# Performance work log

Hardware: AMD Instinct MI355X
Metric: run time of the kernel (lower is better)

The kernel has to match this reference:

```python
import jax, jax.numpy as jnp
import numpy as np

EMBED_DIM = 1024


def setup_inputs() -> dict:
    key = jax.random.key(0)
    ks = jax.random.split(key, 9)
    d = EMBED_DIM
    s = 1.0 / np.sqrt(d)
    x = jax.random.normal(ks[0], (4, 4096, d), dtype=jnp.float32)
    Wq = jax.random.normal(ks[1], (d, d), dtype=jnp.float32) * s
    bq = jax.random.normal(ks[2], (d,), dtype=jnp.float32) * 0.01
    Wk = jax.random.normal(ks[3], (d, d), dtype=jnp.float32) * s
    bk = jax.random.normal(ks[4], (d,), dtype=jnp.float32) * 0.01
    Wv = jax.random.normal(ks[5], (d, d), dtype=jnp.float32) * s
    bv = jax.random.normal(ks[6], (d,), dtype=jnp.float32) * 0.01
    Wo = jax.random.normal(ks[7], (d, d), dtype=jnp.float32) * s
    bo = jax.random.normal(ks[8], (d,), dtype=jnp.float32) * 0.01
    return {"x": x, "Wq": Wq, "bq": bq, "Wk": Wk, "bk": bk,
            "Wv": Wv, "bv": bv, "Wo": Wo, "bo": bo}


def reference(x, Wq, bq, Wk, bk, Wv, bv, Wo, bo):
    # x: [b, s, d]; single-head attention, scale = 1/sqrt(d)
    b, s, d = x.shape
    q = x @ Wq + bq
    k = x @ Wk + bk
    v = x @ Wv + bv
    scale = 1.0 / jnp.sqrt(jnp.asarray(d, x.dtype))
    scores = jnp.einsum('bqd,bkd->bqk', q, k) * scale  # [b, s, s]
    causal = jnp.tril(jnp.ones((s, s), dtype=bool))
    scores = jnp.where(causal, scores, jnp.asarray(-jnp.inf, scores.dtype))
    attn = jax.nn.softmax(scores, axis=-1)
    ctx = jnp.einsum('bqk,bkd->bqd', attn, v)
    return ctx @ Wo + bo
```

## Files before the change

### kernel.cpp

```cpp
#include <hip/hip_runtime.h>


typedef unsigned short u16;
typedef __attribute__((ext_vector_type(4))) unsigned short u16x4;
typedef __attribute__((ext_vector_type(8))) unsigned short u16x8;
typedef __attribute__((ext_vector_type(8))) __bf16 bf16x8;
typedef __attribute__((ext_vector_type(4))) float f32x4;

typedef const __attribute__((address_space(1))) void* as1cp;
typedef __attribute__((address_space(3))) void* as3p;

template <int N> struct IC { static constexpr int v = N; };

struct GemmPtrs {
  const u16* A[4];
  const u16* B[4];
  const float* bias[4];
  void* C[4];
};
struct TransPtrs {
  const void* in[4];
  u16* out[4];
};
struct SmPtrs {
  u16* P[4];
};

__device__ __forceinline__ u16 f2bf(float f) {
  union { float f; unsigned int i; } c; c.f = f;
  unsigned int r = c.i + 0x7fffu + ((c.i >> 16) & 1u);
  return (u16)(r >> 16);
}
__device__ __forceinline__ float bf2f(u16 u) {
  union { unsigned int i; float f; } c; c.i = ((unsigned int)u) << 16;
  return c.f;
}

__global__ __launch_bounds__(256) void cast_f32_bf16(const float* __restrict__ in,
                                                     u16* __restrict__ out, int n4) {
  int i = blockIdx.x * blockDim.x + threadIdx.x;
  if (i >= n4) return;
  float4 v = ((const float4*)in)[i];
  u16x4 u;
  u.x = f2bf(v.x); u.y = f2bf(v.y); u.z = f2bf(v.z); u.w = f2bf(v.w);
  ((u16x4*)out)[i] = u;
}

template <bool IN_F32>
__global__ __launch_bounds__(256) void transpose_to_bf16(TransPtrs tp, int R, int C) {
  __shared__ u16 t[32][34];
  int z = blockIdx.z;
  int tx = threadIdx.x, ty = threadIdx.y;
  int c0 = blockIdx.x * 32, r0 = blockIdx.y * 32;
#pragma unroll
  for (int dy = 0; dy < 4; ++dy) {
    int r = r0 + ty + dy * 8;
    int c = c0 + tx;
    u16 hv;
    if (IN_F32) hv = f2bf(((const float*)tp.in[z])[(size_t)r * C + c]);
    else        hv = ((const u16*)tp.in[z])[(size_t)r * C + c];
    t[ty + dy * 8][tx] = hv;
  }
  __syncthreads();
  u16* op = tp.out[z];
#pragma unroll
  for (int dy = 0; dy < 4; ++dy) {
    int a = ty + dy * 8;
    op[(size_t)(c0 + a) * R + r0 + tx] = t[tx][a];
  }
}

__global__ __launch_bounds__(256) void softmax_causal(SmPtrs sp) {
  int row = blockIdx.x;
  u16* P = sp.P[blockIdx.y];
  int tid = threadIdx.x;
  int lane = tid & 63, wv = tid >> 6;
  u16x8* prow = (u16x8*)(P + (size_t)row * 4096);
  int nch = (row >> 3) + 1;
  int fend = ((row >> 7) + 1) << 4;
  int c0 = tid, c1 = tid + 256;
  bool a0 = c0 < nch, a1 = c1 < nch;
  float vals[16];
  float lmax = -3.0e38f;
  if (a0) {
    u16x8 u = prow[c0];
#pragma unroll
    for (int e = 0; e < 8; ++e) {
      float f = (c0 * 8 + e <= row) ? bf2f(u[e]) : -3.0e38f;
      vals[e] = f; lmax = fmaxf(lmax, f);
    }
  } else {
#pragma unroll
    for (int e = 0; e < 8; ++e) vals[e] = -3.0e38f;
  }
  if (a1) {
    u16x8 u = prow[c1];
#pragma unroll
    for (int e = 0; e < 8; ++e) {
      float f = (c1 * 8 + e <= row) ? bf2f(u[e]) : -3.0e38f;
      vals[8 + e] = f; lmax = fmaxf(lmax, f);
    }
  } else {
#pragma unroll
    for (int e = 0; e < 8; ++e) vals[8 + e] = -3.0e38f;
  }
  __shared__ float red[8];
#pragma unroll
  for (int off = 32; off > 0; off >>= 1) lmax = fmaxf(lmax, __shfl_down(lmax, off, 64));
  if (lane == 0) red[wv] = lmax;
  __syncthreads();
  float m2 = fmaxf(fmaxf(red[0], red[1]), fmaxf(red[2], red[3]));
  float lsum = 0.f;
#pragma unroll
  for (int e = 0; e < 16; ++e) {
    float ev = __expf(vals[e] - m2);
    vals[e] = ev;
    lsum += ev;
  }
#pragma unroll
  for (int off = 32; off > 0; off >>= 1) lsum += __shfl_down(lsum, off, 64);
  if (lane == 0) red[4 + wv] = lsum;
  __syncthreads();
  float inv = 1.0f / (red[4] + red[5] + red[6] + red[7]);
  if (a0) {
    u16x8 u;
#pragma unroll
    for (int e = 0; e < 8; ++e) u[e] = f2bf(vals[e] * inv);
    prow[c0] = u;
  }
  if (a1) {
    u16x8 u;
#pragma unroll
    for (int e = 0; e < 8; ++e) u[e] = f2bf(vals[8 + e] * inv);
    prow[c1] = u;
  }
  u16x8 zz = (u16x8)(u16)0;
  for (int c = nch + tid; c < fend; c += 256) prow[c] = zz;
}

template <int MODE, bool OUT_BF16, bool HAS_BIAS>
__global__ __launch_bounds__(512, 2) void gemm256p(GemmPtrs p, int N, float cscale) {
  __shared__ __align__(16) u16 As[4][8192];
  __shared__ __align__(16) u16 Bs[4][8192];
  const int b = blockIdx.x;
  const int tid = threadIdx.x, lane = tid & 63, wv = tid >> 6;
  const int wm = (wv >> 2) << 7, wn = (wv & 3) << 6;
  const int lrow = lane & 15, lquad = lane >> 4;
  const int xs = (lquad ^ ((lrow >> 1) & 3)) << 3;
  const int aoff0 = (wm + lrow) * 32 + xs;
  const int boff0 = (wn + lrow) * 32 + xs;
  const int soff = (tid >> 2) * 1024 + (((tid & 3) ^ ((tid >> 3) & 3)) << 3);
  const int x = b & 7, u = b >> 3;
  const int nslot = (MODE == 1) ? (u < 4 ? 3 : 2) : (MODE == 0 ? 3 : 1);

  struct TP { const u16* A; const u16* B; int tm, tn, z; };
  auto tileOf = [&](int s) {
    TP t;
    if (MODE == 0) {
      int i = x * 32 + u;
      t.z = s; t.tm = (i >> 2) << 8; t.tn = (i & 3) << 8;
    } else if (MODE == 1) {
      int g = x * 68 + s * 32 + u;
      t.z = g / 136; int L = g - t.z * 136;
      int i = (int)((__fsqrt_rn(8.f * (float)L + 1.f) - 1.f) * 0.5f);
      while ((i + 1) * (i + 2) / 2 <= L) ++i;
      while (i * (i + 1) / 2 > L) --i;
      t.tm = i << 8; t.tn = (L - ((i * (i + 1)) >> 1)) << 8;
    } else {
      int i = x * 32 + u;
      t.z = 0; t.tm = (i >> 2) << 8; t.tn = (i & 3) << 8;
    }
    t.A = p.A[t.z] + (size_t)t.tm * 1024;
    t.B = p.B[t.z] + (size_t)t.tn * 1024;
    return t;
  };

  const u16* gA; const u16* gB; int stk = 0, sslot = 0;
  {
    TP t0 = tileOf(0);
    gA = t0.A + soff; gB = t0.B + soff;
  }
  auto adv = [&]() {
    gA += 32; gB += 32;
    ++stk;
    if (stk == 32 && sslot < nslot) {
      stk = 0; ++sslot;
      if (sslot < nslot) {
        TP t = tileOf(sslot);
        gA = t.A + soff; gB = t.B + soff;
      }
    }
  };

  f32x4 acc[8][4];
#pragma unroll
  for (int i = 0; i < 8; ++i)
#pragma unroll
    for (int j = 0; j < 4; ++j) acc[i][j] = (f32x4){0.f, 0.f, 0.f, 0.f};

  bf16x8 alo[4], ahi[4], bg0[4], bg1[4];

#pragma unroll
  for (int pt = 0; pt < 3; ++pt) {
    __builtin_amdgcn_global_load_lds((as1cp)gA, (as3p)(As[pt] + wv * 512), 16, 0, 0);
    __builtin_amdgcn_global_load_lds((as1cp)(gA + 131072), (as3p)(As[pt] + 4096 + wv * 512), 16, 0, 0);
    __builtin_amdgcn_global_load_lds((as1cp)gB, (as3p)(Bs[pt] + wv * 512), 16, 0, 0);
    __builtin_amdgcn_global_load_lds((as1cp)(gB + 131072), (as3p)(Bs[pt] + 4096 + wv * 512), 16, 0, 0);
    adv();
  }
  asm volatile("s_waitcnt vmcnt(8)" ::: "memory");
  asm volatile("s_barrier" ::: "memory");
#pragma unroll
  for (int m = 0; m < 4; ++m) alo[m] = *(const bf16x8*)&As[0][aoff0 + m * 512];
#pragma unroll
  for (int n = 0; n < 4; ++n) bg0[n] = *(const bf16x8*)&Bs[0][boff0 + n * 512];

  auto kt = [&](auto CC, auto SS, auto VV, auto& BU, auto& BL)
      __attribute__((always_inline)) {
    constexpr int c = decltype(CC)::v;
    constexpr int stg = decltype(SS)::v;
    constexpr int vm = decltype(VV)::v;
    __builtin_amdgcn_s_setprio(1);
#pragma unroll
    for (int m = 0; m < 4; ++m)
#pragma unroll
      for (int n = 0; n < 4; ++n)
        acc[m][n] = __builtin_amdgcn_mfma_f32_16x16x32_bf16(alo[m], BU[n], acc[m][n], 0, 0, 0);
    __builtin_amdgcn_s_setprio(0);
#pragma unroll
    for (int m = 0; m < 4; ++m)
      ahi[m] = *(const bf16x8*)&As[c][aoff0 + 2048 + m * 512];
    if constexpr (stg) {
      __builtin_amdgcn_global_load_lds((as1cp)gA, (as3p)(As[(c + 3) & 3] + wv * 512), 16, 0, 0);
      __builtin_amdgcn_global_load_lds((as1cp)(gA + 131072), (as3p)(As[(c + 3) & 3] + 4096 + wv * 512), 16, 0, 0);
    }
    if constexpr (vm == 6) asm volatile("s_waitcnt vmcnt(6)" ::: "memory");
    else if constexpr (vm == 4) asm volatile("s_waitcnt vmcnt(4)" ::: "memory");
    else if constexpr (vm == 0) asm volatile("s_waitcnt vmcnt(0)" ::: "memory");
    asm volatile("s_barrier" ::: "memory");
    __builtin_amdgcn_s_setprio(1);
#pragma unroll
    for (int m = 0; m < 4; ++m)
#pragma unroll
      for (int n = 0; n < 4; ++n)
        acc[4 + m][n] = __builtin_amdgcn_mfma_f32_16x16x32_bf16(ahi[m], BU[n], acc[4 + m][n], 0, 0, 0);
    __builtin_amdgcn_s_setprio(0);
#pragma unroll
    for (int m = 0; m < 4; ++m)
      alo[m] = *(const bf16x8*)&As[(c + 1) & 3][aoff0 + m * 512];
#pragma unroll
    for (int n = 0; n < 4; ++n)
      BL[n] = *(const bf16x8*)&Bs[(c + 1) & 3][boff0 + n * 512];
    if constexpr (stg) {
      __builtin_amdgcn_global_load_lds((as1cp)gB, (as3p)(Bs[(c + 3) & 3] + wv * 512), 16, 0, 0);
      __builtin_amdgcn_global_load_lds((as1cp)(gB + 131072), (as3p)(Bs[(c + 3) & 3] + 4096 + wv * 512), 16, 0, 0);
      adv();
    }
    asm volatile("s_barrier" ::: "memory");
  };

  auto epi = [&](int cs2) {
    TP t = tileOf(cs2);
    float bvv[4] = {0.f, 0.f, 0.f, 0.f};
    if constexpr (HAS_BIAS) {
#pragma unroll
      for (int n = 0; n < 4; ++n) bvv[n] = p.bias[t.z][t.tn + wn + n * 16 + lrow];
    }
#pragma unroll
    for (int m = 0; m < 8; ++m)
#pragma unroll
      for (int r = 0; r < 4; ++r) {
        size_t row = (size_t)(t.tm + wm + m * 16 + lquad * 4 + r);
#pragma unroll
        for (int n = 0; n < 4; ++n) {
          int col = t.tn + wn + n * 16 + lrow;
          float vvv = acc[m][n][r] * cscale + bvv[n];
          if (OUT_BF16) ((u16*)p.C[t.z])[row * N + col] = f2bf(vvv);
          else          ((float*)p.C[t.z])[row * N + col] = vvv;
        }
      }
#pragma unroll
    for (int m2 = 0; m2 < 8; ++m2)
#pragma unroll
      for (int n2 = 0; n2 < 4; ++n2) acc[m2][n2] = (f32x4){0.f, 0.f, 0.f, 0.f};
  };

  const int total = nslot * 32;
  int cs = 0;
  for (int G = 0; G + 4 < total; G += 4) {
    kt(IC<0>{}, IC<1>{}, IC<6>{}, bg0, bg1);
    kt(IC<1>{}, IC<1>{}, IC<6>{}, bg1, bg0);
    kt(IC<2>{}, IC<1>{}, IC<6>{}, bg0, bg1);
    kt(IC<3>{}, IC<1>{}, IC<6>{}, bg1, bg0);
    if (((G + 4) & 31) == 0) { epi(cs); ++cs; }
  }
  kt(IC<0>{}, IC<1>{}, IC<6>{}, bg0, bg1);
  kt(IC<1>{}, IC<0>{}, IC<4>{}, bg1, bg0);
  kt(IC<2>{}, IC<0>{}, IC<0>{}, bg0, bg1);
  kt(IC<3>{}, IC<0>{}, IC<-1>{}, bg1, bg0);
  epi(nslot - 1);
}

__global__ __launch_bounds__(512, 2) void gemm_pv(GemmPtrs p) {
  __shared__ __align__(16) u16 As[4][4096];
  __shared__ __align__(16) u16 Bs[4][8192];
  const int b = blockIdx.x;
  const int tid = threadIdx.x, lane = tid & 63, wv = tid >> 6;
  const int wm = (wv >> 2) << 6, wn = (wv & 3) << 6;
  const int lrow = lane & 15, lquad = lane >> 4;
  const int xs = (lquad ^ ((lrow >> 1) & 3)) << 3;
  const int aoff0 = (wm + lrow) * 32 + xs;
  const int boff0 = (wn + lrow) * 32 + xs;
  const int soff = (tid >> 2) * 4096 + (((tid & 3) ^ ((tid >> 3) & 3)) << 3);
  const int x = b & 7, u = b >> 3;
  const int P = x * 32 + u;
  const int z = P >> 6, j = (P >> 2) & 15, n4 = P & 3;
  const int i1 = j, i2 = 31 - j;
  const int tn = n4 << 8;
  const int T1 = (i1 + 1) * 4;
  const int niter1 = (i2 + 1) * 4;
  const u16* Abase = p.A[z];
  const u16* Bbase = p.B[z] + (size_t)tn * 4096;

  const u16* gA = Abase + (size_t)(i1 << 7) * 4096 + soff;
  const u16* gB = Bbase + soff;
  int stk = 0, sslot = 0;
  auto adv = [&]() {
    gA += 32; gB += 32;
    ++stk;
    if (sslot == 0 && stk == T1) {
      stk = 0; sslot = 1;
      gA = Abase + (size_t)(i2 << 7) * 4096 + soff;
      gB = Bbase + soff;
    } else if (sslot == 1 && stk == niter1) {
      stk = 0; sslot = 2;
    }
  };

  f32x4 acc[4][4];
#pragma unroll
  for (int i = 0; i < 4; ++i)
#pragma unroll
    for (int jj = 0; jj < 4; ++jj) acc[i][jj] = (f32x4){0.f, 0.f, 0.f, 0.f};

  bf16x8 a0[4], a1[4], b0[4], b1[4];

  auto stage = [&](int slot) __attribute__((always_inline)) {
    __builtin_amdgcn_global_load_lds((as1cp)gA, (as3p)(As[slot] + wv * 512), 16, 0, 0);
    __builtin_amdgcn_global_load_lds((as1cp)gB, (as3p)(Bs[slot] + wv * 512), 16, 0, 0);
    __builtin_amdgcn_global_load_lds((as1cp)(gB + 524288), (as3p)(Bs[slot] + 4096 + wv * 512), 16, 0, 0);
    adv();
  };

  stage(0); stage(1); stage(2);
  asm volatile("s_waitcnt vmcnt(3)" ::: "memory");
  asm volatile("s_barrier" ::: "memory");
#pragma unroll
  for (int m = 0; m < 4; ++m) a0[m] = *(const bf16x8*)&As[0][aoff0 + m * 512];
#pragma unroll
  for (int n = 0; n < 4; ++n) b0[n] = *(const bf16x8*)&Bs[0][boff0 + n * 512];

  auto kt = [&](auto CC, auto SS, auto VV, auto& AU, auto& BU, auto& AL, auto& BL)
      __attribute__((always_inline)) {
    constexpr int c = decltype(CC)::v;
    constexpr int stg = decltype(SS)::v;
    constexpr int vm = decltype(VV)::v;
    __builtin_amdgcn_s_setprio(1);
#pragma unroll
    for (int m = 0; m < 4; ++m)
#pragma unroll
      for (int n = 0; n < 4; ++n)
        acc[m][n] = __builtin_amdgcn_mfma_f32_16x16x32_bf16(AU[m], BU[n], acc[m][n], 0, 0, 0);
    __builtin_amdgcn_s_setprio(0);
#pragma unroll
    for (int m = 0; m < 4; ++m)
      AL[m] = *(const bf16x8*)&As[(c + 1) & 3][aoff0 + m * 512];
#pragma unroll
    for (int n = 0; n < 4; ++n)
      BL[n] = *(const bf16x8*)&Bs[(c + 1) & 3][boff0 + n * 512];
    if constexpr (stg) stage((c + 3) & 3);
    if constexpr (vm == 3) asm volatile("s_waitcnt vmcnt(3)" ::: "memory");
    else if constexpr (vm == 0) asm volatile("s_waitcnt vmcnt(0)" ::: "memory");
    asm volatile("s_barrier" ::: "memory");
  };

  auto epi = [&](int s) {
    int tm = (s ? i2 : i1) << 7;
#pragma unroll
    for (int m = 0; m < 4; ++m)
#pragma unroll
      for (int r = 0; r < 4; ++r) {
        size_t row = (size_t)(tm + wm + m * 16 + lquad * 4 + r);
#pragma unroll
        for (int n = 0; n < 4; ++n) {
          int col = tn + wn + n * 16 + lrow;
          ((u16*)p.C[z])[row * 1024 + col] = f2bf(acc[m][n][r]);
        }
      }
#pragma unroll
    for (int m2 = 0; m2 < 4; ++m2)
#pragma unroll
      for (int n2 = 0; n2 < 4; ++n2) acc[m2][n2] = (f32x4){0.f, 0.f, 0.f, 0.f};
  };

  const int total = 132;
  for (int G = 0; G + 4 < total; G += 4) {
    kt(IC<0>{}, IC<1>{}, IC<3>{}, a0, b0, a1, b1);
    kt(IC<1>{}, IC<1>{}, IC<3>{}, a1, b1, a0, b0);
    kt(IC<2>{}, IC<1>{}, IC<3>{}, a0, b0, a1, b1);
    kt(IC<3>{}, IC<1>{}, IC<3>{}, a1, b1, a0, b0);
    if (G + 4 == T1) epi(0);
  }
  kt(IC<0>{}, IC<1>{}, IC<3>{}, a0, b0, a1, b1);
  kt(IC<1>{}, IC<0>{}, IC<3>{}, a1, b1, a0, b0);
  kt(IC<2>{}, IC<0>{}, IC<0>{}, a0, b0, a1, b1);
  kt(IC<3>{}, IC<0>{}, IC<-1>{}, a1, b1, a0, b0);
  epi(1);
}

extern "C" void kernel_launch(void* const* d_in, const int* in_sizes, int n_in,
                              void* d_out, int out_size, void* d_ws, size_t ws_size,
                              hipStream_t stream) {
  const float* x  = (const float*)d_in[0];
  const float* Wq = (const float*)d_in[1];
  const float* bq = (const float*)d_in[2];
  const float* Wk = (const float*)d_in[3];
  const float* bk = (const float*)d_in[4];
  const float* Wv = (const float*)d_in[5];
  const float* bv = (const float*)d_in[6];
  const float* Wo = (const float*)d_in[7];
  const float* bo = (const float*)d_in[8];

  const int S = 4096, D = 1024;
  const size_t XE = (size_t)4 * S * D;
  const size_t BSE = (size_t)S * D;

  char* ws = (char*)d_ws;
  u16* xb  = (u16*)(ws + 0);
  u16* q   = (u16*)(ws + 33554432);
  u16* k   = (u16*)(ws + 67108864);
  u16* v   = (u16*)(ws + 100663296);
  u16* ctx = (u16*)(ws + 134217728);
  u16* wqT = (u16*)(ws + 167772160);
  u16* wkT = wqT + 1048576;
  u16* wvT = wkT + 1048576;
  u16* woT = wvT + 1048576;
  u16* attn2 = (u16*)(ws + 176160768);
  u16* attn0 = (u16*)d_out;
  u16* attn1 = attn0 + (size_t)S * S;
  u16* attn3 = v;
  u16* vT = xb;
  u16* attn[4] = {attn0, attn1, attn2, attn3};

  cast_f32_bf16<<<(int)(XE / 4 / 256), 256, 0, stream>>>(x, xb, (int)(XE / 4));
  {
    TransPtrs tp = {{Wq, Wk, Wv, Wo}, {wqT, wkT, wvT, woT}};
    transpose_to_bf16<true><<<dim3(32, 32, 4), dim3(32, 8), 0, stream>>>(tp, D, D);
  }
  {
    GemmPtrs gp = {{xb, xb, xb, xb}, {wqT, wkT, wvT, wqT},
                   {bq, bk, bv, bq}, {q, k, v, q}};
    gemm256p<0, true, true><<<256, 512, 0, stream>>>(gp, D, 1.0f);
  }
  {
    TransPtrs tp = {{v, v + BSE, v + 2 * BSE, v + 3 * BSE},
                    {vT, vT + BSE, vT + 2 * BSE, vT + 3 * BSE}};
    transpose_to_bf16<false><<<dim3(D / 32, S / 32, 4), dim3(32, 8), 0, stream>>>(tp, S, D);
  }
  {
    GemmPtrs gp = {{q, q + BSE, q + 2 * BSE, q + 3 * BSE},
                   {k, k + BSE, k + 2 * BSE, k + 3 * BSE},
                   {nullptr, nullptr, nullptr, nullptr},
                   {attn[0], attn[1], attn[2], attn[3]}};
    gemm256p<1, true, false><<<256, 512, 0, stream>>>(gp, S, 0.03125f);
  }
  {
    SmPtrs sp = {{attn[0], attn[1], attn[2], attn[3]}};
    softmax_causal<<<dim3(S, 4), 256, 0, stream>>>(sp);
  }
  {
    GemmPtrs gp = {{attn[0], attn[1], attn[2], attn[3]},
                   {vT, vT + BSE, vT + 2 * BSE, vT + 3 * BSE},
                   {nullptr, nullptr, nullptr, nullptr},
                   {ctx, ctx + BSE, ctx + 2 * BSE, ctx + 3 * BSE}};
    gemm_pv<<<256, 512, 0, stream>>>(gp);
  }
  {
    GemmPtrs gp = {{ctx, ctx, ctx, ctx}, {woT, woT, woT, woT},
                   {bo, bo, bo, bo}, {d_out, d_out, d_out, d_out}};
    gemm256p<3, false, true><<<256, 512, 0, stream>>>(gp, D, 1.0f);
  }
}
```

Measured before the change: 522.4 us.

## Switch GEMM kernels to K=64 double-buffered pipeline with 8-chunk XOR swizzle

Rewrites the main GEMM and the PV GEMM main loops. The old 4-stage K=32 ring with hand-scheduled fragment prefetch becomes a 2-stage K=64 double buffer, using a wider 8-way XOR swizzle and one barrier pair per step. This halves the number of barrier and waitcnt sync points per K and simplifies scheduling. The cost is a shallower prefetch depth, so global-load latency is hidden less, and LDS fragment reads are no longer overlapped with MFMAs from the previous step.

After: 518.7 us. No clear change (-0.7%).

```diff
diff --git a/kernel.cpp b/kernel.cpp
--- a/kernel.cpp
+++ b/kernel.cpp
@@ -10,7 +10,8 @@
 typedef const __attribute__((address_space(1))) void* as1cp;
 typedef __attribute__((address_space(3))) void* as3p;
 
-template <int N> struct IC { static constexpr int v = N; };
+#define SBAR() __builtin_amdgcn_s_barrier()
+#define SPIN() __builtin_amdgcn_sched_barrier(0)
 
 struct GemmPtrs {
   const u16* A[4];
@@ -139,17 +140,19 @@
 }
 
 template <int MODE, bool OUT_BF16, bool HAS_BIAS>
-__global__ __launch_bounds__(512, 2) void gemm256p(GemmPtrs p, int N, float cscale) {
-  __shared__ __align__(16) u16 As[4][8192];
-  __shared__ __align__(16) u16 Bs[4][8192];
+__global__ __launch_bounds__(512, 2) void gemm256q(GemmPtrs p, int N, float cscale) {
+  __shared__ __align__(16) u16 As[2][16384];
+  __shared__ __align__(16) u16 Bs[2][16384];
   const int b = blockIdx.x;
   const int tid = threadIdx.x, lane = tid & 63, wv = tid >> 6;
   const int wm = (wv >> 2) << 7, wn = (wv & 3) << 6;
   const int lrow = lane & 15, lquad = lane >> 4;
-  const int xs = (lquad ^ ((lrow >> 1) & 3)) << 3;
-  const int aoff0 = (wm + lrow) * 32 + xs;
-  const int boff0 = (wn + lrow) * 32 + xs;
-  const int soff = (tid >> 2) * 1024 + (((tid & 3) ^ ((tid >> 3) & 3)) << 3);
+  const int xsw = lrow & 7;
+  const int ch0 = (lquad ^ xsw) << 3;
+  const int ch1 = ((4 + lquad) ^ xsw) << 3;
+  const int arow = (wm + lrow) * 64;
+  const int brow = (wn + lrow) * 64;
+  const int soff = (tid >> 3) * 1024 + (((tid & 7) ^ ((tid >> 3) & 7)) << 3);
   const int x = b & 7, u = b >> 3;
   const int nslot = (MODE == 1) ? (u < 4 ? 3 : 2) : (MODE == 0 ? 3 : 1);
 
@@ -181,83 +184,32 @@
     gA = t0.A + soff; gB = t0.B + soff;
   }
   auto adv = [&]() {
-    gA += 32; gB += 32;
-    ++stk;
-    if (stk == 32 && sslot < nslot) {
-      stk = 0; ++sslot;
-      if (sslot < nslot) {
+    gA += 64; gB += 64;
+    if (++stk == 16) {
+      stk = 0;
+      if (++sslot < nslot) {
         TP t = tileOf(sslot);
         gA = t.A + soff; gB = t.B + soff;
       }
     }
   };
+  auto stage = [&](int sb) __attribute__((always_inline)) {
+#pragma unroll
+    for (int L = 0; L < 4; ++L)
+      __builtin_amdgcn_global_load_lds((as1cp)(gA + L * 65536),
+                                       (as3p)(As[sb] + (tid + L * 512) * 8), 16, 0, 0);
+#pragma unroll
+    for (int L = 0; L < 4; ++L)
+      __builtin_amdgcn_global_load_lds((as1cp)(gB + L * 65536),
+                                       (as3p)(Bs[sb] + (tid + L * 512) * 8), 16, 0, 0);
+    adv();
+  };
 
   f32x4 acc[8][4];
 #pragma unroll
   for (int i = 0; i < 8; ++i)
 #pragma unroll
     for (int j = 0; j < 4; ++j) acc[i][j] = (f32x4){0.f, 0.f, 0.f, 0.f};
-
-  bf16x8 alo[4], ahi[4], bg0[4], bg1[4];
-
-#pragma unroll
-  for (int pt = 0; pt < 3; ++pt) {
-    __builtin_amdgcn_global_load_lds((as1cp)gA, (as3p)(As[pt] + wv * 512), 16, 0, 0);
-    __builtin_amdgcn_global_load_lds((as1cp)(gA + 131072), (as3p)(As[pt] + 4096 + wv * 512), 16, 0, 0);
-    __builtin_amdgcn_global_load_lds((as1cp)gB, (as3p)(Bs[pt] + wv * 512), 16, 0, 0);
-    __builtin_amdgcn_global_load_lds((as1cp)(gB + 131072), (as3p)(Bs[pt] + 4096 + wv * 512), 16, 0, 0);
-    adv();
-  }
-  asm volatile("s_waitcnt vmcnt(8)" ::: "memory");
-  asm volatile("s_barrier" ::: "memory");
-#pragma unroll
-  for (int m = 0; m < 4; ++m) alo[m] = *(const bf16x8*)&As[0][aoff0 + m * 512];
-#pragma unroll
-  for (int n = 0; n < 4; ++n) bg0[n] = *(const bf16x8*)&Bs[0][boff0 + n * 512];
-
-  auto kt = [&](auto CC, auto SS, auto VV, auto& BU, auto& BL)
-      __attribute__((always_inline)) {
-    constexpr int c = decltype(CC)::v;
-    constexpr int stg = decltype(SS)::v;
-    constexpr int vm = decltype(VV)::v;
-    __builtin_amdgcn_s_setprio(1);
-#pragma unroll
-    for (int m = 0; m < 4; ++m)
-#pragma unroll
-      for (int n = 0; n < 4; ++n)
-        acc[m][n] = __builtin_amdgcn_mfma_f32_16x16x32_bf16(alo[m], BU[n], acc[m][n], 0, 0, 0);
-    __builtin_amdgcn_s_setprio(0);
-#pragma unroll
-    for (int m = 0; m < 4; ++m)
-      ahi[m] = *(const bf16x8*)&As[c][aoff0 + 2048 + m * 512];
-    if constexpr (stg) {
-      __builtin_amdgcn_global_load_lds((as1cp)gA, (as3p)(As[(c + 3) & 3] + wv * 512), 16, 0, 0);
-      __builtin_amdgcn_global_load_lds((as1cp)(gA + 131072), (as3p)(As[(c + 3) & 3] + 4096 + wv * 512), 16, 0, 0);
-    }
-    if constexpr (vm == 6) asm volatile("s_waitcnt vmcnt(6)" ::: "memory");
-    else if constexpr (vm == 4) asm volatile("s_waitcnt vmcnt(4)" ::: "memory");
-    else if constexpr (vm == 0) asm volatile("s_waitcnt vmcnt(0)" ::: "memory");
-    asm volatile("s_barrier" ::: "memory");
-    __builtin_amdgcn_s_setprio(1);
-#pragma unroll
-    for (int m = 0; m < 4; ++m)
-#pragma unroll
-      for (int n = 0; n < 4; ++n)
-        acc[4 + m][n] = __builtin_amdgcn_mfma_f32_16x16x32_bf16(ahi[m], BU[n], acc[4 + m][n], 0, 0, 0);
-    __builtin_amdgcn_s_setprio(0);
-#pragma unroll
-    for (int m = 0; m < 4; ++m)
-      alo[m] = *(const bf16x8*)&As[(c + 1) & 3][aoff0 + m * 512];
-#pragma unroll
-    for (int n = 0; n < 4; ++n)
-      BL[n] = *(const bf16x8*)&Bs[(c + 1) & 3][boff0 + n * 512];
-    if constexpr (stg) {
-      __builtin_amdgcn_global_load_lds((as1cp)gB, (as3p)(Bs[(c + 3) & 3] + wv * 512), 16, 0, 0);
-      __builtin_amdgcn_global_load_lds((as1cp)(gB + 131072), (as3p)(Bs[(c + 3) & 3] + 4096 + wv * 512), 16, 0, 0);
-      adv();
-    }
-    asm volatile("s_barrier" ::: "memory");
-  };
 
   auto epi = [&](int cs2) {
     TP t = tileOf(cs2);
@@ -285,56 +237,111 @@
       for (int n2 = 0; n2 < 4; ++n2) acc[m2][n2] = (f32x4){0.f, 0.f, 0.f, 0.f};
   };
 
-  const int total = nslot * 32;
+  stage(0);
+  asm volatile("s_waitcnt vmcnt(0)");
+  SBAR();
+  SPIN();
+
+  const int T = nslot * 16;
   int cs = 0;
-  for (int G = 0; G + 4 < total; G += 4) {
-    kt(IC<0>{}, IC<1>{}, IC<6>{}, bg0, bg1);
-    kt(IC<1>{}, IC<1>{}, IC<6>{}, bg1, bg0);
-    kt(IC<2>{}, IC<1>{}, IC<6>{}, bg0, bg1);
-    kt(IC<3>{}, IC<1>{}, IC<6>{}, bg1, bg0);
-    if (((G + 4) & 31) == 0) { epi(cs); ++cs; }
-  }
-  kt(IC<0>{}, IC<1>{}, IC<6>{}, bg0, bg1);
-  kt(IC<1>{}, IC<0>{}, IC<4>{}, bg1, bg0);
-  kt(IC<2>{}, IC<0>{}, IC<0>{}, bg0, bg1);
-  kt(IC<3>{}, IC<0>{}, IC<-1>{}, bg1, bg0);
-  epi(nslot - 1);
-}
-
-__global__ __launch_bounds__(512, 2) void gemm_pv(GemmPtrs p) {
-  __shared__ __align__(16) u16 As[4][4096];
-  __shared__ __align__(16) u16 Bs[4][8192];
+  for (int t = 0; t < T; ++t) {
+    const int cb = t & 1;
+    if (t + 1 < T) {
+      stage(cb ^ 1);
+      SPIN();
+      asm volatile("s_waitcnt vmcnt(8)");
+    } else {
+      SPIN();
+      asm volatile("s_waitcnt vmcnt(0)");
+    }
+    SBAR();
+    SPIN();
+    __builtin_amdgcn_s_setprio(1);
+    {
+      bf16x8 af[4], bf[4];
+#pragma unroll
+      for (int m = 0; m < 4; ++m) af[m] = *(const bf16x8*)&As[cb][arow + m * 1024 + ch0];
+#pragma unroll
+      for (int n = 0; n < 4; ++n) bf[n] = *(const bf16x8*)&Bs[cb][brow + n * 1024 + ch0];
+#pragma unroll
+      for (int m = 0; m < 4; ++m)
+#pragma unroll
+        for (int n = 0; n < 4; ++n)
+          acc[m][n] = __builtin_amdgcn_mfma_f32_16x16x32_bf16(af[m], bf[n], acc[m][n], 0, 0, 0);
+#pragma unroll
+      for (int m = 0; m < 4; ++m) af[m] = *(const bf16x8*)&As[cb][arow + 4096 + m * 1024 + ch0];
+#pragma unroll
+      for (int m = 0; m < 4; ++m)
+#pragma unroll
+        for (int n = 0; n < 4; ++n)
+          acc[4 + m][n] = __builtin_amdgcn_mfma_f32_16x16x32_bf16(af[m], bf[n], acc[4 + m][n], 0, 0, 0);
+#pragma unroll
+      for (int m = 0; m < 4; ++m) af[m] = *(const bf16x8*)&As[cb][arow + 4096 + m * 1024 + ch1];
+#pragma unroll
+      for (int n = 0; n < 4; ++n) bf[n] = *(const bf16x8*)&Bs[cb][brow + n * 1024 + ch1];
+#pragma unroll
+      for (int m = 0; m < 4; ++m)
+#pragma unroll
+        for (int n = 0; n < 4; ++n)
+          acc[4 + m][n] = __builtin_amdgcn_mfma_f32_16x16x32_bf16(af[m], bf[n], acc[4 + m][n], 0, 0, 0);
+#pragma unroll
+      for (int m = 0; m < 4; ++m) af[m] = *(const bf16x8*)&As[cb][arow + m * 1024 + ch1];
+#pragma unroll
+      for (int m = 0; m < 4; ++m)
+#pragma unroll
+        for (int n = 0; n < 4; ++n)
+          acc[m][n] = __builtin_amdgcn_mfma_f32_16x16x32_bf16(af[m], bf[n], acc[m][n], 0, 0, 0);
+    }
+    __builtin_amdgcn_s_setprio(0);
+    SBAR();
+    SPIN();
+    if (((t + 1) & 15) == 0) { epi(cs); ++cs; }
+  }
+}
+
+__global__ __launch_bounds__(512, 2) void gemm_pv64(GemmPtrs p) {
+  __shared__ __align__(16) u16 As[2][8192];
+  __shared__ __align__(16) u16 Bs[2][16384];
   const int b = blockIdx.x;
   const int tid = threadIdx.x, lane = tid & 63, wv = tid >> 6;
   const int wm = (wv >> 2) << 6, wn = (wv & 3) << 6;
   const int lrow = lane & 15, lquad = lane >> 4;
-  const int xs = (lquad ^ ((lrow >> 1) & 3)) << 3;
-  const int aoff0 = (wm + lrow) * 32 + xs;
-  const int boff0 = (wn + lrow) * 32 + xs;
-  const int soff = (tid >> 2) * 4096 + (((tid & 3) ^ ((tid >> 3) & 3)) << 3);
+  const int xsw = lrow & 7;
+  const int ch0 = (lquad ^ xsw) << 3;
+  const int ch1 = ((4 + lquad) ^ xsw) << 3;
+  const int arow = (wm + lrow) * 64;
+  const int brow = (wn + lrow) * 64;
+  const int soff = (tid >> 3) * 4096 + (((tid & 7) ^ ((tid >> 3) & 7)) << 3);
   const int x = b & 7, u = b >> 3;
   const int P = x * 32 + u;
   const int z = P >> 6, j = (P >> 2) & 15, n4 = P & 3;
   const int i1 = j, i2 = 31 - j;
   const int tn = n4 << 8;
-  const int T1 = (i1 + 1) * 4;
-  const int niter1 = (i2 + 1) * 4;
+  const int T1 = 2 * (i1 + 1);
+  const int T = 66;
   const u16* Abase = p.A[z];
   const u16* Bbase = p.B[z] + (size_t)tn * 4096;
 
   const u16* gA = Abase + (size_t)(i1 << 7) * 4096 + soff;
   const u16* gB = Bbase + soff;
-  int stk = 0, sslot = 0;
+  int stk = 0;
   auto adv = [&]() {
-    gA += 32; gB += 32;
-    ++stk;
-    if (sslot == 0 && stk == T1) {
-      stk = 0; sslot = 1;
+    gA += 64; gB += 64;
+    if (++stk == T1) {
       gA = Abase + (size_t)(i2 << 7) * 4096 + soff;
       gB = Bbase + soff;
-    } else if (sslot == 1 && stk == niter1) {
-      stk = 0; sslot = 2;
-    }
+    }
+  };
+  auto stage = [&](int sb) __attribute__((always_inline)) {
+#pragma unroll
+    for (int L = 0; L < 2; ++L)
+      __builtin_amdgcn_global_load_lds((as1cp)(gA + (size_t)L * 262144),
+                                       (as3p)(As[sb] + (tid + L * 512) * 8), 16, 0, 0);
+#pragma unroll
+    for (int L = 0; L < 4; ++L)
+      __builtin_amdgcn_global_load_lds((as1cp)(gB + (size_t)L * 262144),
+                                       (as3p)(Bs[sb] + (tid + L * 512) * 8), 16, 0, 0);
+    adv();
   };
 
   f32x4 acc[4][4];
@@ -342,47 +349,6 @@
   for (int i = 0; i < 4; ++i)
 #pragma unroll
     for (int jj = 0; jj < 4; ++jj) acc[i][jj] = (f32x4){0.f, 0.f, 0.f, 0.f};
-
-  bf16x8 a0[4], a1[4], b0[4], b1[4];
-
-  auto stage = [&](int slot) __attribute__((always_inline)) {
-    __builtin_amdgcn_global_load_lds((as1cp)gA, (as3p)(As[slot] + wv * 512), 16, 0, 0);
-    __builtin_amdgcn_global_load_lds((as1cp)gB, (as3p)(Bs[slot] + wv * 512), 16, 0, 0);
-    __builtin_amdgcn_global_load_lds((as1cp)(gB + 524288), (as3p)(Bs[slot] + 4096 + wv * 512), 16, 0, 0);
-    adv();
-  };
-
-  stage(0); stage(1); stage(2);
-  asm volatile("s_waitcnt vmcnt(3)" ::: "memory");
-  asm volatile("s_barrier" ::: "memory");
-#pragma unroll
-  for (int m = 0; m < 4; ++m) a0[m] = *(const bf16x8*)&As[0][aoff0 + m * 512];
-#pragma unroll
-  for (int n = 0; n < 4; ++n) b0[n] = *(const bf16x8*)&Bs[0][boff0 + n * 512];
-
-  auto kt = [&](auto CC, auto SS, auto VV, auto& AU, auto& BU, auto& AL, auto& BL)
-      __attribute__((always_inline)) {
-    constexpr int c = decltype(CC)::v;
-    constexpr int stg = decltype(SS)::v;
-    constexpr int vm = decltype(VV)::v;
-    __builtin_amdgcn_s_setprio(1);
-#pragma unroll
-    for (int m = 0; m < 4; ++m)
-#pragma unroll
-      for (int n = 0; n < 4; ++n)
-        acc[m][n] = __builtin_amdgcn_mfma_f32_16x16x32_bf16(AU[m], BU[n], acc[m][n], 0, 0, 0);
-    __builtin_amdgcn_s_setprio(0);
-#pragma unroll
-    for (int m = 0; m < 4; ++m)
-      AL[m] = *(const bf16x8*)&As[(c + 1) & 3][aoff0 + m * 512];
-#pragma unroll
-    for (int n = 0; n < 4; ++n)
-      BL[n] = *(const bf16x8*)&Bs[(c + 1) & 3][boff0 + n * 512];
-    if constexpr (stg) stage((c + 3) & 3);
-    if constexpr (vm == 3) asm volatile("s_waitcnt vmcnt(3)" ::: "memory");
-    else if constexpr (vm == 0) asm volatile("s_waitcnt vmcnt(0)" ::: "memory");
-    asm volatile("s_barrier" ::: "memory");
-  };
 
   auto epi = [&](int s) {
     int tm = (s ? i2 : i1) << 7;
@@ -403,18 +369,50 @@
       for (int n2 = 0; n2 < 4; ++n2) acc[m2][n2] = (f32x4){0.f, 0.f, 0.f, 0.f};
   };
 
-  const int total = 132;
-  for (int G = 0; G + 4 < total; G += 4) {
-    kt(IC<0>{}, IC<1>{}, IC<3>{}, a0, b0, a1, b1);
-    kt(IC<1>{}, IC<1>{}, IC<3>{}, a1, b1, a0, b0);
-    kt(IC<2>{}, IC<1>{}, IC<3>{}, a0, b0, a1, b1);
-    kt(IC<3>{}, IC<1>{}, IC<3>{}, a1, b1, a0, b0);
-    if (G + 4 == T1) epi(0);
-  }
-  kt(IC<0>{}, IC<1>{}, IC<3>{}, a0, b0, a1, b1);
-  kt(IC<1>{}, IC<0>{}, IC<3>{}, a1, b1, a0, b0);
-  kt(IC<2>{}, IC<0>{}, IC<0>{}, a0, b0, a1, b1);
-  kt(IC<3>{}, IC<0>{}, IC<-1>{}, a1, b1, a0, b0);
+  stage(0);
+  asm volatile("s_waitcnt vmcnt(0)");
+  SBAR();
+  SPIN();
+
+  for (int t = 0; t < T; ++t) {
+    const int cb = t & 1;
+    if (t + 1 < T) {
+      stage(cb ^ 1);
+      SPIN();
+      asm volatile("s_waitcnt vmcnt(6)");
+    } else {
+      SPIN();
+      asm volatile("s_waitcnt vmcnt(0)");
+    }
+    SBAR();
+    SPIN();
+    __builtin_amdgcn_s_setprio(1);
+    {
+      bf16x8 af[4], bf[4];
+#pragma unroll
+      for (int m = 0; m < 4; ++m) af[m] = *(const bf16x8*)&As[cb][arow + m * 1024 + ch0];
+#pragma unroll
+      for (int n = 0; n < 4; ++n) bf[n] = *(const bf16x8*)&Bs[cb][brow + n * 1024 + ch0];
+#pragma unroll
+      for (int m = 0; m < 4; ++m)
+#pragma unroll
+        for (int n = 0; n < 4; ++n)
+          acc[m][n] = __builtin_amdgcn_mfma_f32_16x16x32_bf16(af[m], bf[n], acc[m][n], 0, 0, 0);
+#pragma unroll
+      for (int m = 0; m < 4; ++m) af[m] = *(const bf16x8*)&As[cb][arow + m * 1024 + ch1];
+#pragma unroll
+      for (int n = 0; n < 4; ++n) bf[n] = *(const bf16x8*)&Bs[cb][brow + n * 1024 + ch1];
+#pragma unroll
+      for (int m = 0; m < 4; ++m)
+#pragma unroll
+        for (int n = 0; n < 4; ++n)
+          acc[m][n] = __builtin_amdgcn_mfma_f32_16x16x32_bf16(af[m], bf[n], acc[m][n], 0, 0, 0);
+    }
+    __builtin_amdgcn_s_setprio(0);
+    SBAR();
+    SPIN();
+    if (t + 1 == T1) epi(0);
+  }
   epi(1);
 }
 
@@ -460,7 +458,7 @@
   {
     GemmPtrs gp = {{xb, xb, xb, xb}, {wqT, wkT, wvT, wqT},
                    {bq, bk, bv, bq}, {q, k, v, q}};
-    gemm256p<0, true, true><<<256, 512, 0, stream>>>(gp, D, 1.0f);
+    gemm256q<0, true, true><<<256, 512, 0, stream>>>(gp, D, 1.0f);
   }
   {
     TransPtrs tp = {{v, v + BSE, v + 2 * BSE, v + 3 * BSE},
@@ -472,7 +470,7 @@
                    {k, k + BSE, k + 2 * BSE, k + 3 * BSE},
                    {nullptr, nullptr, nullptr, nullptr},
                    {attn[0], attn[1], attn[2], attn[3]}};
-    gemm256p<1, true, false><<<256, 512, 0, stream>>>(gp, S, 0.03125f);
+    gemm256q<1, true, false><<<256, 512, 0, stream>>>(gp, S, 0.03125f);
   }
   {
     SmPtrs sp = {{attn[0], attn[1], attn[2], attn[3]}};
@@ -483,11 +481,11 @@
                    {vT, vT + BSE, vT + 2 * BSE, vT + 3 * BSE},
                    {nullptr, nullptr, nullptr, nullptr},
                    {ctx, ctx + BSE, ctx + 2 * BSE, ctx + 3 * BSE}};
-    gemm_pv<<<256, 512, 0, stream>>>(gp);
+    gemm_pv64<<<256, 512, 0, stream>>>(gp);
   }
   {
     GemmPtrs gp = {{ctx, ctx, ctx, ctx}, {woT, woT, woT, woT},
                    {bo, bo, bo, bo}, {d_out, d_out, d_out, d_out}};
-    gemm256p<3, false, true><<<256, 512, 0, stream>>>(gp, D, 1.0f);
-  }
-}
+    gemm256q<3, false, true><<<256, 512, 0, stream>>>(gp, D, 1.0f);
+  }
+}
```
